# Performance work log

Hardware: AMD Instinct MI355X
Metric: run time of the kernel (lower is better)

The kernel has to match this reference:

```python
import jax, jax.numpy as jnp
import numpy as np
import math

B, T, D_MODEL, N_HEADS = 4, 2048, 1024, 16
HEAD_DIM = D_MODEL // N_HEADS


def setup_inputs() -> dict:
    key = jax.random.key(0)
    k1, k2, k3 = jax.random.split(key, 3)
    x = jax.random.normal(k1, (B, T, D_MODEL), dtype=jnp.float32)
    # torch Linear weight layout: [out_features, in_features]
    w_qkv = jax.random.normal(k2, (3 * D_MODEL, D_MODEL), dtype=jnp.float32) * (1.0 / math.sqrt(D_MODEL))
    w_out = jax.random.normal(k3, (D_MODEL, D_MODEL), dtype=jnp.float32) * (1.0 / math.sqrt(D_MODEL))
    return {"x": x, "w_qkv": w_qkv, "w_out": w_out}


def reference(x, w_qkv, w_out):
    b, t, c = x.shape
    h, d = N_HEADS, HEAD_DIM
    # qkv projection: (B,T,3C) -> (3,B,H,T,D)
    qkv = jnp.einsum('btc,fc->btf', x, w_qkv)
    qkv = qkv.reshape(b, t, 3, h, d).transpose(2, 0, 3, 1, 4)
    q, k, v = qkv[0], qkv[1], qkv[2]
    scale = 1.0 / math.sqrt(d)
    # full O(T^2) attention scores, causal masked
    scores = jnp.einsum('bhqd,bhkd->bhqk', q, k) * scale
    causal = jnp.tril(jnp.ones((t, t), dtype=bool))
    scores = jnp.where(causal[None, None, :, :], scores, jnp.float32(-jnp.inf))
    attn = jax.nn.softmax(scores, axis=-1)
    out = jnp.einsum('bhqk,bhkd->bhqd', attn, v)  # (B,H,T,D)
    out = out.transpose(0, 2, 1, 3).reshape(b, t, c)
    out = jnp.einsum('btc,oc->bto', out, w_out)
    return out
```

## Files before the change

### kernel.cpp

```cpp
#include <hip/hip_runtime.h>
#include <hip/hip_bf16.h>

#define T_SEQ 2048
#define BATCH 4
#define NH    16
#define DM    1024
#define HD    64

typedef __attribute__((ext_vector_type(4))) float  f32x4;
typedef __attribute__((ext_vector_type(8))) short  s16x8;
typedef __attribute__((ext_vector_type(4))) short  s16x4;

__device__ __forceinline__ unsigned short f2b(float f) {
  union { float f; unsigned u; } v; v.f = f;
  unsigned u = v.u;
  unsigned r = 0x7fffu + ((u >> 16) & 1u);
  u += r;
  return (unsigned short)(u >> 16);
}

__device__ __forceinline__ f32x4 mfma16(s16x8 a, s16x8 b, f32x4 c) {
  return __builtin_amdgcn_mfma_f32_16x16x32_bf16(a, b, c, 0, 0, 0);
}

__device__ __forceinline__ float exp2_fast(float x) {
  float r; asm("v_exp_f32 %0, %1" : "=v"(r) : "v"(x)); return r;
}

__device__ __forceinline__ unsigned cvt_pk_bf16(float lo, float hi) {
  unsigned r; asm("v_cvt_pk_bf16_f32 %0, %1, %2" : "=v"(r) : "v"(lo), "v"(hi)); return r;
}

#define BAR() __builtin_amdgcn_s_barrier()
#define SCB() __builtin_amdgcn_sched_barrier(0)
#define LGK(n) do { asm volatile("s_waitcnt lgkmcnt(" #n ")" ::: "memory"); SCB(); } while (0)
#define VMC(n) do { asm volatile("s_waitcnt vmcnt(" #n ")" ::: "memory"); } while (0)

__global__ void cvt_all(const float* __restrict__ x, const float* __restrict__ wq,
                        const float* __restrict__ wo,
                        unsigned short* __restrict__ xb, unsigned short* __restrict__ wqb,
                        unsigned short* __restrict__ wob) {
  const int N4X = (BATCH * T_SEQ * DM) / 4;
  const int N4Q = (3 * DM * DM) / 4;
  const int N4O = (DM * DM) / 4;
  const int N4QSCALED = (DM * DM) / 4;
  int i = blockIdx.x * blockDim.x + threadIdx.x;
  int stride = gridDim.x * blockDim.x;
  for (int j = i; j < N4X + N4Q + N4O; j += stride) {
    const float* src; unsigned short* dst; int k; float scale = 1.f;
    if (j < N4X) { src = x; dst = xb; k = j; }
    else if (j < N4X + N4Q) {
      k = j - N4X; src = wq; dst = wqb;
      if (k < N4QSCALED) scale = 0.18033688011112042f;
    } else { k = j - N4X - N4Q; src = wo; dst = wob; }
    f32x4 v = ((const f32x4*)src)[k];
    s16x4 o;
    o.x = (short)f2b(v.x * scale); o.y = (short)f2b(v.y * scale);
    o.z = (short)f2b(v.z * scale); o.w = (short)f2b(v.w * scale);
    ((s16x4*)dst)[k] = o;
  }
}

__device__ __forceinline__ void rd4(s16x8 (&d)[4], const char* base, int rbase, int cb) {
#pragma unroll
  for (int j = 0; j < 4; ++j)
    d[j] = *(const s16x8*)(base + (rbase + j * 16) * 128 + cb);
}

__device__ __forceinline__ void stage_half(const unsigned short* __restrict__ Msrc,
                                           int rt0, int kt, char* lbase, int half,
                                           int srow8, int c2src, int c2lin, int Kd) {
#pragma unroll
  for (int q = 0; q < 2; ++q) {
    int rl = half * 128 + q * 64 + srow8;
    const char* src = (const char*)(Msrc + (size_t)(rt0 + rl) * Kd + kt) + c2src;
    __builtin_amdgcn_global_load_lds((const void*)src, (void*)(lbase + rl * 128 + c2lin),
                                     16, 0, 0);
  }
}

__device__ __forceinline__ void clust(f32x4 (&acc)[8][4], const s16x8 (&a)[4],
                                      const s16x8 (&b)[4], int mb) {
  __builtin_amdgcn_s_setprio(1);
#pragma unroll
  for (int j = 0; j < 4; ++j)
#pragma unroll
    for (int n = 0; n < 4; ++n)
      acc[mb + j][n] = mfma16(a[j], b[n], acc[mb + j][n]);
  __builtin_amdgcn_s_setprio(0);
}

template<int OUTF32>
__global__ __launch_bounds__(512, 2)
void gemm8p(const unsigned short* __restrict__ A, const unsigned short* __restrict__ B,
            void* __restrict__ C, int M, int N, int K) {
  __shared__ char smem[131072];
  char* A0b = smem;
  char* A1b = smem + 32768;
  char* B0b = smem + 65536;
  char* B1b = smem + 98304;

  const int tid = threadIdx.x;
  const int lane = tid & 63;
  const int w = tid >> 6;
  const int wm = w >> 2, wn = w & 3;
  const int lr = lane & 15, g = lane >> 4;

  const int gx = gridDim.x, nwg = gx * gridDim.y;
  const int bid = blockIdx.y * gx + blockIdx.x;
  const int cpx = nwg >> 3;
  const int b2 = (bid & 7) * cpx + (bid >> 3);
  const int row0 = (b2 % gx) * 256;
  const int col0 = (b2 / gx) * 256;

  const int srow8 = tid >> 3;
  const int c2lin = (tid & 7) * 16;
  const int c2src = ((tid & 7) ^ (srow8 & 7)) * 16;

  const int swz = (lr & 7) << 4;
  const int cs0 = (g * 16) ^ swz;
  const int cs1 = (64 + g * 16) ^ swz;
  const int rAlo = wm * 128 + lr;
  const int rAhi = rAlo + 64;
  const int rB = wn * 64 + lr;

  f32x4 acc[8][4] = {};
  s16x8 aP[4], aQ[4], aR[4], bP[4], bQ[4];

  const int NT = K / 64;

  stage_half(A, row0, 0, A0b, 0, srow8, c2src, c2lin, K);
  stage_half(A, row0, 0, A0b, 1, srow8, c2src, c2lin, K);
  stage_half(B, col0, 0, B0b, 0, srow8, c2src, c2lin, K);
  stage_half(B, col0, 0, B0b, 1, srow8, c2src, c2lin, K);
  stage_half(A, row0, 64, A1b, 0, srow8, c2src, c2lin, K);
  VMC(2);
  BAR();
  rd4(aP, A0b, rAlo, cs0);
  rd4(bP, B0b, rB, cs0);

  auto body = [&](char* Ac, char* Bc, char* An, char* Bn, int t) {
    const int ktn  = min(t + 1, NT - 1) * 64;
    const int ktn2 = min(t + 2, NT - 1) * 64;
    rd4(aQ, Ac, rAhi, cs0);
    stage_half(A, row0, ktn, An, 1, srow8, c2src, c2lin, K);
    BAR(); LGK(4);
    clust(acc, aP, bP, 0);
    BAR();
    rd4(aP, Ac, rAlo, cs1);
    rd4(aR, Ac, rAhi, cs1);
    rd4(bQ, Bc, rB, cs1);
    stage_half(B, col0, ktn, Bn, 0, srow8, c2src, c2lin, K);
    BAR(); LGK(12);
    clust(acc, aQ, bP, 4);
    BAR();
    stage_half(B, col0, ktn, Bn, 1, srow8, c2src, c2lin, K);
    BAR(); LGK(0);
    clust(acc, aP, bQ, 0);
    BAR();
    stage_half(A, row0, ktn2, Ac, 0, srow8, c2src, c2lin, K);
    VMC(2);
    BAR();
    rd4(aP, An, rAlo, cs0);
    rd4(bP, Bn, rB, cs0);
    clust(acc, aR, bQ, 4);
    BAR();
  };

#pragma unroll 1
  for (int tt = 0; tt < NT; tt += 2) {
    body(A0b, B0b, A1b, B1b, tt);
    body(A1b, B1b, A0b, B0b, tt + 1);
  }

#pragma unroll
  for (int m = 0; m < 8; ++m)
#pragma unroll
    for (int n = 0; n < 4; ++n)
#pragma unroll
      for (int i = 0; i < 4; ++i) {
        int row = row0 + wm * 128 + m * 16 + g * 4 + i;
        int col = col0 + wn * 64 + n * 16 + lr;
        if (OUTF32)
          ((float*)C)[(size_t)row * N + col] = acc[m][n][i];
        else
          ((unsigned short*)C)[(size_t)row * N + col] = f2b(acc[m][n][i]);
      }
}

__global__ __launch_bounds__(512)
void attn_kernel(const unsigned short* __restrict__ qkv,
                 unsigned short* __restrict__ out) {
  __shared__ unsigned short Ks[2][64 * 64];
  __shared__ unsigned short Vt[2][64 * 72];
  __shared__ unsigned short Ps[8][16 * 72];

  const int tid  = threadIdx.x;
  const int lane = tid & 63;
  const int w    = tid >> 6;
  const int lr   = lane & 15, g = lane >> 4;
  const int bid  = blockIdx.x;
  const int bh   = bid & 63;
  const int pi   = bid >> 6;
  const int b    = bh >> 4, h = bh & 15;
  const size_t rb = (size_t)b * T_SEQ;

  const bool grpV = (tid < 256);
  const int vd0 = (tid & 7) * 8, vr0 = (tid >> 3) * 2;
  const int t2  = tid - 256;
  const int kr0 = t2 >> 3, kc0 = t2 & 7;

#pragma unroll 1
  for (int ph = 0; ph < 2; ++ph) {
    const int qt = ph ? (15 - pi) : pi;
    const int q0 = qt * 128;
    const int qr = q0 + w * 16;
    const int qq = qr + lr;
    const int nt = 2 * qt + 2;
    const int qmax = qr + 15;

    s16x8 qf[2];
    {
      const unsigned short* qp = qkv + (rb + qq) * 3072 + h * 64;
      qf[0] = *(const s16x8*)(qp + g * 8);
      qf[1] = *(const s16x8*)(qp + 32 + g * 8);
    }

    float mI = -1e30f, lI = 0.f;
    f32x4 o[4] = {};

    s16x8 pre0, pre1;
    {
      if (grpV) {
        const unsigned short* vp = &qkv[(rb + vr0) * 3072 + 2048 + h * 64 + vd0];
        pre0 = *(const s16x8*)vp;
        pre1 = *(const s16x8*)(vp + 3072);
      } else {
        const unsigned short* kp = &qkv[(rb + kr0) * 3072 + 1024 + h * 64 + kc0 * 8];
        pre0 = *(const s16x8*)kp;
        pre1 = *(const s16x8*)(kp + 32 * 3072);
      }
    }

    for (int t = 0; t < nt; ++t) {
      const int cur = t & 1;
      if (grpV) {
#pragma unroll
        for (int jj = 0; jj < 8; ++jj) {
          int d = vd0 + jj;
          int sw = ((d ^ (d >> 3)) & 7) << 4;
          unsigned val = (unsigned)(unsigned short)pre0[jj] |
                         ((unsigned)(unsigned short)pre1[jj] << 16);
          *(unsigned*)((char*)&Vt[cur][0] + d * 144 + ((vr0 * 2) ^ sw)) = val;
        }
      } else {
        *(s16x8*)((char*)&Ks[cur][0] + kr0 * 128 + ((kc0 * 16) ^ ((kr0 & 7) << 4))) = pre0;
        int kr1 = kr0 + 32;
        *(s16x8*)((char*)&Ks[cur][0] + kr1 * 128 + ((kc0 * 16) ^ ((kr1 & 7) << 4))) = pre1;
      }
      __syncthreads();

      if (t + 1 < nt) {
        const int kv0n = (t + 1) * 64;
        if (grpV) {
          const unsigned short* vp = &qkv[(rb + kv0n + vr0) * 3072 + 2048 + h * 64 + vd0];
          pre0 = *(const s16x8*)vp;
          pre1 = *(const s16x8*)(vp + 3072);
        } else {
          const unsigned short* kp = &qkv[(rb + kv0n + kr0) * 3072 + 1024 + h * 64 + kc0 * 8];
          pre0 = *(const s16x8*)kp;
          pre1 = *(const s16x8*)(kp + 32 * 3072);
        }
      }

      const int kv0 = t * 64;
      if (kv0 <= qmax) {
        f32x4 s4[4];
        __builtin_amdgcn_s_setprio(1);
#pragma unroll
        for (int kc = 0; kc < 4; ++kc) {
          int row = kc * 16 + lr;
          const char* kbase = (const char*)&Ks[cur][0] + row * 128;
          int sw = (row & 7) << 4;
          s16x8 kf0 = *(const s16x8*)(kbase + ((g * 16) ^ sw));
          s16x8 kf1 = *(const s16x8*)(kbase + ((64 + g * 16) ^ sw));
          f32x4 s = {};
          s = mfma16(kf0, qf[0], s);
          s = mfma16(kf1, qf[1], s);
          s4[kc] = s;
        }
        __builtin_amdgcn_s_setprio(0);

        if (kv0 + 63 > qr) {
#pragma unroll
          for (int kc = 0; kc < 4; ++kc)
#pragma unroll
            for (int i = 0; i < 4; ++i) {
              int key = kv0 + kc * 16 + g * 4 + i;
              if (key > qq) s4[kc][i] = -1e30f;
            }
        }

        float mx = fmaxf(fmaxf(fmaxf(s4[0][0], s4[0][1]), fmaxf(s4[0][2], s4[0][3])),
                   fmaxf(fmaxf(fmaxf(s4[1][0], s4[1][1]), fmaxf(s4[1][2], s4[1][3])),
                   fmaxf(fmaxf(fmaxf(s4[2][0], s4[2][1]), fmaxf(s4[2][2], s4[2][3])),
                         fmaxf(fmaxf(s4[3][0], s4[3][1]), fmaxf(s4[3][2], s4[3][3])))));
        mx = fmaxf(mx, __shfl_xor(mx, 16));
        mx = fmaxf(mx, __shfl_xor(mx, 32));

        const bool defer = __all(mx - mI <= 11.5f);
        float alpha;
        if (defer) {
          alpha = 1.f;
        } else {
          float mn = fmaxf(mI, mx);
          alpha = exp2_fast(mI - mn);
          mI = mn;
        }
        float rs = 0.f;
#pragma unroll
        for (int kc = 0; kc < 4; ++kc)
#pragma unroll
          for (int i = 0; i < 4; ++i) {
            float p = exp2_fast(s4[kc][i] - mI);
            s4[kc][i] = p;
            rs += p;
          }
        rs += __shfl_xor(rs, 16);
        rs += __shfl_xor(rs, 32);
        lI = lI * alpha + rs;

        {
          char* pw = (char*)&Ps[w][0] + lr * 144;
#pragma unroll
          for (int kc = 0; kc < 4; ++kc) {
            unsigned v0 = cvt_pk_bf16(s4[kc][0], s4[kc][1]);
            unsigned v1 = cvt_pk_bf16(s4[kc][2], s4[kc][3]);
            unsigned long long pv = (unsigned long long)v0 | ((unsigned long long)v1 << 32);
            *(unsigned long long*)(pw + kc * 32 + g * 8) = pv;
          }
        }

        if (!defer) {
#pragma unroll
          for (int n = 0; n < 4; ++n)
#pragma unroll
            for (int i = 0; i < 4; ++i)
              o[n][i] *= alpha;
        }

        asm volatile("s_waitcnt lgkmcnt(0)" ::: "memory");

        __builtin_amdgcn_s_setprio(1);
#pragma unroll
        for (int kk = 0; kk < 2; ++kk) {
          s16x8 pf = *(const s16x8*)((const char*)&Ps[w][0] + lr * 144 + kk * 64 + g * 16);
#pragma unroll
          for (int n = 0; n < 4; ++n) {
            int d = n * 16 + lr;
            int sw = ((d ^ (d >> 3)) & 7) << 4;
            s16x8 vf = *(const s16x8*)((const char*)&Vt[cur][0] + d * 144 + ((kk * 64 + g * 16) ^ sw));
            o[n] = mfma16(vf, pf, o[n]);
          }
        }
        __builtin_amdgcn_s_setprio(0);
      }
    }

    float rl = 1.f / lI;
#pragma unroll
    for (int n = 0; n < 4; ++n) {
      unsigned p0 = cvt_pk_bf16(o[n][0] * rl, o[n][1] * rl);
      unsigned p1 = cvt_pk_bf16(o[n][2] * rl, o[n][3] * rl);
      unsigned long long pv = (unsigned long long)p0 | ((unsigned long long)p1 << 32);
      *(unsigned long long*)&out[(rb + qq) * 1024 + h * 64 + n * 16 + g * 4] = pv;
    }
  }
}

extern "C" void kernel_launch(void* const* d_in, const int* in_sizes, int n_in,
                              void* d_out, int out_size, void* d_ws, size_t ws_size,
                              hipStream_t stream) {
  const float* x     = (const float*)d_in[0];
  const float* w_qkv = (const float*)d_in[1];
  const float* w_out = (const float*)d_in[2];

  const size_t n_x   = (size_t)BATCH * T_SEQ * DM;
  const size_t n_wq  = (size_t)3 * DM * DM;
  const size_t n_wo  = (size_t)DM * DM;
  const size_t n_qkv = (size_t)BATCH * T_SEQ * 3 * DM;
  const size_t need  = (n_x + n_wq + n_wo + n_qkv + n_x) * 2;
  if (ws_size < need) return;

  unsigned short* xb  = (unsigned short*)d_ws;
  unsigned short* wqb = xb + n_x;
  unsigned short* wob = wqb + n_wq;
  unsigned short* qkv = wob + n_wo;
  unsigned short* att = qkv + n_qkv;

  cvt_all<<<2048, 256, 0, stream>>>(x, w_qkv, w_out, xb, wqb, wob);

  gemm8p<0><<<dim3(32, 12), 512, 0, stream>>>(xb, wqb, qkv, BATCH * T_SEQ, 3 * DM, DM);
  attn_kernel<<<512, 512, 0, stream>>>(qkv, att);
  gemm8p<1><<<dim3(32, 4), 512, 0, stream>>>(att, wob, d_out, BATCH * T_SEQ, DM, DM);
}
```

Measured before the change: 186.9 us.

## Use 256x128 output tiles for out-projection GEMM and simplify V-tile swizzle

Adds a template variant of the GEMM that uses a 128-wide N tile, skips the second B half-stage and adjusts the LDS wait counts. The output projection is launched with twice as many workgroups (256 instead of 128), so more of the 256 CUs have work. It also changes the V-transpose LDS swizzle to a simpler XOR pattern, which alters bank-conflict behaviour in attention. The cost is a lower MFMA-to-load ratio per tile and possible new bank conflicts.

New measurement: 177.2 us (median of 3 runs). 5.2% less time.

```diff
diff --git a/kernel.cpp b/kernel.cpp
--- a/kernel.cpp
+++ b/kernel.cpp
@@ -61,9 +61,10 @@
   }
 }
 
-__device__ __forceinline__ void rd4(s16x8 (&d)[4], const char* base, int rbase, int cb) {
-#pragma unroll
-  for (int j = 0; j < 4; ++j)
+template<int NB>
+__device__ __forceinline__ void rdN(s16x8 (&d)[4], const char* base, int rbase, int cb) {
+#pragma unroll
+  for (int j = 0; j < NB; ++j)
     d[j] = *(const s16x8*)(base + (rbase + j * 16) * 128 + cb);
 }
 
@@ -79,21 +80,23 @@
   }
 }
 
+template<int NB>
 __device__ __forceinline__ void clust(f32x4 (&acc)[8][4], const s16x8 (&a)[4],
                                       const s16x8 (&b)[4], int mb) {
   __builtin_amdgcn_s_setprio(1);
 #pragma unroll
   for (int j = 0; j < 4; ++j)
 #pragma unroll
-    for (int n = 0; n < 4; ++n)
+    for (int n = 0; n < NB; ++n)
       acc[mb + j][n] = mfma16(a[j], b[n], acc[mb + j][n]);
   __builtin_amdgcn_s_setprio(0);
 }
 
-template<int OUTF32>
+template<int OUTF32, int BN128>
 __global__ __launch_bounds__(512, 2)
 void gemm8p(const unsigned short* __restrict__ A, const unsigned short* __restrict__ B,
             void* __restrict__ C, int M, int N, int K) {
+  constexpr int NB = BN128 ? 2 : 4;
   __shared__ char smem[131072];
   char* A0b = smem;
   char* A1b = smem + 32768;
@@ -111,7 +114,7 @@
   const int cpx = nwg >> 3;
   const int b2 = (bid & 7) * cpx + (bid >> 3);
   const int row0 = (b2 % gx) * 256;
-  const int col0 = (b2 / gx) * 256;
+  const int col0 = (b2 / gx) * (BN128 ? 128 : 256);
 
   const int srow8 = tid >> 3;
   const int c2lin = (tid & 7) * 16;
@@ -122,7 +125,7 @@
   const int cs1 = (64 + g * 16) ^ swz;
   const int rAlo = wm * 128 + lr;
   const int rAhi = rAlo + 64;
-  const int rB = wn * 64 + lr;
+  const int rB = wn * (NB * 16) + lr;
 
   f32x4 acc[8][4] = {};
   s16x8 aP[4], aQ[4], aR[4], bP[4], bQ[4];
@@ -132,38 +135,39 @@
   stage_half(A, row0, 0, A0b, 0, srow8, c2src, c2lin, K);
   stage_half(A, row0, 0, A0b, 1, srow8, c2src, c2lin, K);
   stage_half(B, col0, 0, B0b, 0, srow8, c2src, c2lin, K);
-  stage_half(B, col0, 0, B0b, 1, srow8, c2src, c2lin, K);
+  if constexpr (!BN128) stage_half(B, col0, 0, B0b, 1, srow8, c2src, c2lin, K);
   stage_half(A, row0, 64, A1b, 0, srow8, c2src, c2lin, K);
   VMC(2);
   BAR();
-  rd4(aP, A0b, rAlo, cs0);
-  rd4(bP, B0b, rB, cs0);
+  rdN<4>(aP, A0b, rAlo, cs0);
+  rdN<NB>(bP, B0b, rB, cs0);
 
   auto body = [&](char* Ac, char* Bc, char* An, char* Bn, int t) {
     const int ktn  = min(t + 1, NT - 1) * 64;
     const int ktn2 = min(t + 2, NT - 1) * 64;
-    rd4(aQ, Ac, rAhi, cs0);
+    rdN<4>(aQ, Ac, rAhi, cs0);
     stage_half(A, row0, ktn, An, 1, srow8, c2src, c2lin, K);
     BAR(); LGK(4);
-    clust(acc, aP, bP, 0);
-    BAR();
-    rd4(aP, Ac, rAlo, cs1);
-    rd4(aR, Ac, rAhi, cs1);
-    rd4(bQ, Bc, rB, cs1);
+    clust<NB>(acc, aP, bP, 0);
+    BAR();
+    rdN<4>(aP, Ac, rAlo, cs1);
+    rdN<4>(aR, Ac, rAhi, cs1);
+    rdN<NB>(bQ, Bc, rB, cs1);
     stage_half(B, col0, ktn, Bn, 0, srow8, c2src, c2lin, K);
-    BAR(); LGK(12);
-    clust(acc, aQ, bP, 4);
-    BAR();
-    stage_half(B, col0, ktn, Bn, 1, srow8, c2src, c2lin, K);
+    BAR();
+    if constexpr (BN128) { LGK(10); } else { LGK(12); }
+    clust<NB>(acc, aQ, bP, 4);
+    BAR();
+    if constexpr (!BN128) stage_half(B, col0, ktn, Bn, 1, srow8, c2src, c2lin, K);
     BAR(); LGK(0);
-    clust(acc, aP, bQ, 0);
+    clust<NB>(acc, aP, bQ, 0);
     BAR();
     stage_half(A, row0, ktn2, Ac, 0, srow8, c2src, c2lin, K);
     VMC(2);
     BAR();
-    rd4(aP, An, rAlo, cs0);
-    rd4(bP, Bn, rB, cs0);
-    clust(acc, aR, bQ, 4);
+    rdN<4>(aP, An, rAlo, cs0);
+    rdN<NB>(bP, Bn, rB, cs0);
+    clust<NB>(acc, aR, bQ, 4);
     BAR();
   };
 
@@ -176,11 +180,11 @@
 #pragma unroll
   for (int m = 0; m < 8; ++m)
 #pragma unroll
-    for (int n = 0; n < 4; ++n)
+    for (int n = 0; n < NB; ++n)
 #pragma unroll
       for (int i = 0; i < 4; ++i) {
         int row = row0 + wm * 128 + m * 16 + g * 4 + i;
-        int col = col0 + wn * 64 + n * 16 + lr;
+        int col = col0 + wn * (NB * 16) + n * 16 + lr;
         if (OUTF32)
           ((float*)C)[(size_t)row * N + col] = acc[m][n][i];
         else
@@ -248,7 +252,7 @@
 #pragma unroll
         for (int jj = 0; jj < 8; ++jj) {
           int d = vd0 + jj;
-          int sw = ((d ^ (d >> 3)) & 7) << 4;
+          int sw = ((d >> 3) & 7) << 4;
           unsigned val = (unsigned)(unsigned short)pre0[jj] |
                          ((unsigned)(unsigned short)pre1[jj] << 16);
           *(unsigned*)((char*)&Vt[cur][0] + d * 144 + ((vr0 * 2) ^ sw)) = val;
@@ -358,7 +362,7 @@
 #pragma unroll
           for (int n = 0; n < 4; ++n) {
             int d = n * 16 + lr;
-            int sw = ((d ^ (d >> 3)) & 7) << 4;
+            int sw = ((d >> 3) & 7) << 4;
             s16x8 vf = *(const s16x8*)((const char*)&Vt[cur][0] + d * 144 + ((kk * 64 + g * 16) ^ sw));
             o[n] = mfma16(vf, pf, o[n]);
           }
@@ -400,7 +404,7 @@
 
   cvt_all<<<2048, 256, 0, stream>>>(x, w_qkv, w_out, xb, wqb, wob);
 
-  gemm8p<0><<<dim3(32, 12), 512, 0, stream>>>(xb, wqb, qkv, BATCH * T_SEQ, 3 * DM, DM);
+  gemm8p<0, 0><<<dim3(32, 12), 512, 0, stream>>>(xb, wqb, qkv, BATCH * T_SEQ, 3 * DM, DM);
   attn_kernel<<<512, 512, 0, stream>>>(qkv, att);
-  gemm8p<1><<<dim3(32, 4), 512, 0, stream>>>(att, wob, d_out, BATCH * T_SEQ, DM, DM);
-}
+  gemm8p<1, 1><<<dim3(32, 8), 512, 0, stream>>>(att, wob, d_out, BATCH * T_SEQ, DM, DM);
+}
```
